# Kernel tuning notes

Hardware: AMD Instinct MI355X
Metric: run time of the kernel (lower is better)

Reference implementation:

```python
import jax, jax.numpy as jnp
import numpy as np

N_NODES = 100000
N_EDGES = 1600000
HIDDEN = 64
IN_CH = 6  # 3 (direction) + 3 (node feature part)
BN_EPS = 1e-5


def setup_inputs() -> dict:
    key = jax.random.key(0)
    ks = jax.random.split(key, 16)
    inp = {
        "x": jax.random.normal(ks[0], (N_NODES, 3), dtype=jnp.float32),
        "pos": jax.random.normal(ks[1], (N_NODES, 3), dtype=jnp.float32),
        "edge_index": jax.random.randint(ks[2], (2, N_EDGES), 0, N_NODES, dtype=jnp.int64),
    }
    dims = [IN_CH, HIDDEN, HIDDEN, HIDDEN]
    for i in range(3):
        din, dout = dims[i], dims[i + 1]
        inp[f"W{i+1}"] = jax.random.normal(ks[3 + 4 * i], (din, dout), dtype=jnp.float32) * (1.0 / np.sqrt(din))
        inp[f"b{i+1}"] = jnp.zeros((dout,), dtype=jnp.float32)
        inp[f"g{i+1}"] = jnp.ones((dout,), dtype=jnp.float32)   # BN gamma
        inp[f"be{i+1}"] = jnp.zeros((dout,), dtype=jnp.float32)  # BN beta
    return inp


def _mlp_layer(h, W, b, g, be):
    # Linear -> ReLU -> BatchNorm1d (training mode, biased variance like torch)
    h = jax.nn.relu(h @ W + b)
    mu = jnp.mean(h, axis=0)
    var = jnp.mean((h - mu) ** 2, axis=0)
    return g * (h - mu) * jax.lax.rsqrt(var + BN_EPS) + be


def reference(x, pos, edge_index, W1, b1, g1, be1, W2, b2, g2, be2, W3, b3, g3, be3):
    n = x.shape[0]
    xp = jnp.concatenate([pos, x], axis=1)             # [N, 3+F]
    src, dst = edge_index[0], edge_index[1]            # j = src, i = dst (PyG source_to_target)
    x_j = xp[src]                                      # [E, 3+F]
    x_i = xp[dst]
    direction = x_j[:, :3] - x_i[:, :3]                # [E, 3]
    # NOTE: source uses torch.norm with no dim => single global scalar norm
    direction = direction / jnp.linalg.norm(direction)
    h = jnp.concatenate([direction, x_i[:, 3:]], axis=-1)  # [E, IN_CH]
    h = _mlp_layer(h, W1, b1, g1, be1)
    h = _mlp_layer(h, W2, b2, g2, be2)
    h = _mlp_layer(h, W3, b3, g3, be3)                 # [E, HIDDEN]
    out = jax.ops.segment_max(h, dst, num_segments=n)  # scatter-max aggregation
    out = jnp.where(jnp.isfinite(out), out, 0.0)       # PyG fills empty segments with 0
    return out
```

## Files before the change

### kernel.cpp

```cpp
#include <hip/hip_runtime.h>
#include <stdint.h>

typedef unsigned short u16;
typedef unsigned int u32;
typedef __attribute__((ext_vector_type(8))) short short8;
typedef __attribute__((ext_vector_type(4))) float floatx4;

#define BN_EPS 1e-5f
#define NPB 64
#define NPB_SHIFT 6
#define NBMAX 2048

__device__ __forceinline__ float bf2f(u16 u) { return __uint_as_float(((unsigned)u) << 16); }
__device__ __forceinline__ u16 f2bf(float f) {
  unsigned u = __float_as_uint(f);
  u += 0x7FFFu + ((u >> 16) & 1u);
  return (u16)(u >> 16);
}

__global__ void k_init(float* __restrict__ stats, u32* __restrict__ bucketTotal) {
  for (int i = threadIdx.x; i < 1024; i += blockDim.x) stats[i] = 0.f;
  for (int i = threadIdx.x; i < NBMAX + 1; i += blockDim.x) bucketTotal[i] = 0u;
}

__global__ void k_norm_hist(const int* __restrict__ ei, const float* __restrict__ pos,
                            int E, int NB, float* __restrict__ stats,
                            u32* __restrict__ bucketTotal) {
  __shared__ u32 lh[NBMAX];
  __shared__ float red[16];
  for (int i = threadIdx.x; i < NB; i += blockDim.x) lh[i] = 0u;
  __syncthreads();
  int tid = blockIdx.x * blockDim.x + threadIdx.x;
  int stride = gridDim.x * blockDim.x;
  float acc = 0.f;
  for (int e = tid; e < E; e += stride) {
    int s = ei[e], d = ei[E + e];
    float d0 = pos[3 * s + 0] - pos[3 * d + 0];
    float d1 = pos[3 * s + 1] - pos[3 * d + 1];
    float d2 = pos[3 * s + 2] - pos[3 * d + 2];
    acc = fmaf(d0, d0, acc);
    acc = fmaf(d1, d1, acc);
    acc = fmaf(d2, d2, acc);
    atomicAdd(&lh[d >> NPB_SHIFT], 1u);
  }
#pragma unroll
  for (int off = 32; off > 0; off >>= 1) acc += __shfl_down(acc, off, 64);
  if ((threadIdx.x & 63) == 0) red[threadIdx.x >> 6] = acc;
  __syncthreads();
  if (threadIdx.x == 0) {
    float s = 0.f;
    for (int w = 0; w < (int)(blockDim.x >> 6); w++) s += red[w];
    atomicAdd(&stats[0], s);
  }
  for (int i = threadIdx.x; i < NB; i += blockDim.x)
    if (lh[i]) atomicAdd(&bucketTotal[i], lh[i]);
}

__global__ void k_scan(const u32* __restrict__ bucketTotal, u32* __restrict__ base,
                       u32* __restrict__ cursor, int NB) {
  int lane = threadIdx.x;
  u32 run = 0;
  for (int b0 = 0; b0 < NB; b0 += 64) {
    int b = b0 + lane;
    u32 v = (b < NB) ? bucketTotal[b] : 0u;
    u32 s = v;
#pragma unroll
    for (int off = 1; off < 64; off <<= 1) {
      u32 t = __shfl_up(s, off, 64);
      if (lane >= off) s += t;
    }
    u32 excl = run + s - v;
    if (b < NB) { base[b] = excl; cursor[b] = excl; }
    run += __shfl(s, 63, 64);
  }
  if (lane == 0) base[NB] = run;
}

__global__ void k_place(const int* __restrict__ ei, int E, int NB,
                        u32* __restrict__ cursor, u32* __restrict__ sorted) {
  __shared__ u32 lh[NBMAX];
  __shared__ u32 lbase[NBMAX];
  for (int i = threadIdx.x; i < NB; i += blockDim.x) lh[i] = 0u;
  __syncthreads();
  int tid = blockIdx.x * blockDim.x + threadIdx.x;
  int stride = gridDim.x * blockDim.x;
  for (int e = tid; e < E; e += stride) atomicAdd(&lh[ei[E + e] >> NPB_SHIFT], 1u);
  __syncthreads();
  for (int i = threadIdx.x; i < NB; i += blockDim.x) {
    u32 c = lh[i];
    lbase[i] = c ? atomicAdd(&cursor[i], c) : 0u;
    lh[i] = 0u;
  }
  __syncthreads();
  for (int e = tid; e < E; e += stride) {
    int d = ei[E + e];
    int b = d >> NPB_SHIFT;
    u32 slot = lbase[b] + atomicAdd(&lh[b], 1u);
    sorted[slot] = ((u32)e << 8) | (u32)(d & (NPB - 1));
  }
}

__global__ __launch_bounds__(256) void k_bucket_max(
    const u32* __restrict__ sorted, const u32* __restrict__ base,
    const u16* __restrict__ h, const float* __restrict__ gsum3,
    const float* __restrict__ gsq3, const float* __restrict__ g3,
    const float* __restrict__ be3, float invE, float* __restrict__ outf, int N) {
  __shared__ u32 tile[NPB * 64];
  for (int i = threadIdx.x; i < NPB * 64; i += blockDim.x) tile[i] = 0u;
  int b = blockIdx.x;
  u32 start = base[b];
  int cnt = (int)(base[b + 1] - start);
  int t = threadIdx.x;
  int es = t >> 3;
  int c0 = (t & 7) * 8;
  u32 mm[4];
#pragma unroll
  for (int p = 0; p < 4; p++) {
    u32 m0 = (g3[c0 + 2 * p] < 0.f) ? 0xFFFFu : 0u;
    u32 m1 = (g3[c0 + 2 * p + 1] < 0.f) ? 0xFFFFu : 0u;
    mm[p] = m0 | (m1 << 16);
  }
  __syncthreads();

  for (int i0 = 0; i0 < cnt; i0 += 128) {
    uint4 raw[4];
    u32 ln[4];
    int ok[4];
#pragma unroll
    for (int u_ = 0; u_ < 4; u_++) {
      int sl = i0 + u_ * 32 + es;
      ok[u_] = sl < cnt;
      if (ok[u_]) {
        ln[u_] = sorted[start + sl] & (u32)(NPB - 1);
        raw[u_] = *(const uint4*)(h + (long)(start + sl) * 64 + c0);
      }
    }
#pragma unroll
    for (int u_ = 0; u_ < 4; u_++) {
      if (!ok[u_]) continue;
      unsigned w[4] = {raw[u_].x, raw[u_].y, raw[u_].z, raw[u_].w};
      u32 key[8];
#pragma unroll
      for (int p = 0; p < 4; p++) {
        u32 wx = w[p] ^ mm[p];
        key[2 * p] = (wx & 0xFFFFu) | 0x10000u;
        key[2 * p + 1] = (wx >> 16) | 0x10000u;
      }
      u32 baseA = ln[u_] * 64u + (u32)c0;
#pragma unroll
      for (int jj = 0; jj < 8; jj++) {
        int j = (jj + es) & 7;
        atomicMax(&tile[baseA + j], key[j]);
      }
    }
  }
  __syncthreads();
  int c = t & 63;
  float mu = gsum3[c] * invE;
  float var = gsq3[c] * invE - mu * mu;
  float sc = g3[c] * rsqrtf(var + BN_EPS);
  float sh = be3[c] - mu * sc;
  u32 me = (g3[c] < 0.f) ? 0xFFFFu : 0u;
  int node0 = b * NPB;
  for (int l = t; l < NPB * 64; l += blockDim.x) {
    int node = node0 + (l >> 6);
    if (node < N) {
      u32 k = tile[l];
      float v = (k == 0u) ? 0.f : fmaf(bf2f((u16)((k & 0xFFFFu) ^ me)), sc, sh);
      outf[(long)node * 64 + (l & 63)] = v;
    }
  }
}

__global__ __launch_bounds__(256) void k_layer1(
    const int* __restrict__ ei, const float* __restrict__ pos,
    const float* __restrict__ x, const float* __restrict__ W1,
    const float* __restrict__ b1, u16* __restrict__ h,
    const float* __restrict__ stats, float* __restrict__ gsum,
    float* __restrict__ gsq, int E, const u32* __restrict__ sorted) {
  __shared__ float in6[6][256];
  __shared__ float ssum[64], ssq[64];
  float invn = 1.0f / sqrtf(stats[0]);
  int t = threadIdx.x;
  int lane = t & 63;
  int wv = t >> 6;
  float w[6];
#pragma unroll
  for (int k = 0; k < 6; k++) w[k] = W1[k * 64 + lane];
  float bias = b1[lane];
  float psum = 0.f, psq = 0.f;

  int chunks = (E + 255) >> 8;
  for (int c = blockIdx.x; c < chunks; c += gridDim.x) {
    long e0 = (long)c << 8;
    int e = (int)e0 + t;
    float v[6] = {0.f, 0.f, 0.f, 0.f, 0.f, 0.f};
    if (e < E) {
      int eid = sorted ? (int)(sorted[e] >> 8) : e;
      int s = ei[eid], d = ei[E + eid];
      float p0 = pos[3 * s + 0], p1 = pos[3 * s + 1], p2 = pos[3 * s + 2];
      float q0 = pos[3 * d + 0], q1 = pos[3 * d + 1], q2 = pos[3 * d + 2];
      v[0] = (p0 - q0) * invn;
      v[1] = (p1 - q1) * invn;
      v[2] = (p2 - q2) * invn;
      v[3] = x[3 * d + 0];
      v[4] = x[3 * d + 1];
      v[5] = x[3 * d + 2];
    }
    __syncthreads();
#pragma unroll
    for (int k = 0; k < 6; k++) in6[k][t] = v[k];
    __syncthreads();
    int lim = E - (int)e0;
    if (lim > 256) lim = 256;
    int base = wv * 64;
#pragma unroll 4
    for (int i = 0; i < 64; i++) {
      int el = base + i;
      if (el >= lim) break;
      float acc = bias;
#pragma unroll
      for (int k = 0; k < 6; k++) acc = fmaf(in6[k][el], w[k], acc);
      acc = fmaxf(acc, 0.f);
      u16 hb = f2bf(acc);
      h[(e0 + el) * 64 + lane] = hb;
      float hf = bf2f(hb);
      psum += hf;
      psq = fmaf(hf, hf, psq);
    }
  }
  if (t < 64) { ssum[t] = 0.f; ssq[t] = 0.f; }
  __syncthreads();
  atomicAdd(&ssum[lane], psum);
  atomicAdd(&ssq[lane], psq);
  __syncthreads();
  if (t < 64) {
    atomicAdd(&gsum[t], ssum[t]);
    atomicAdd(&gsq[t], ssq[t]);
  }
}

__global__ __launch_bounds__(256) void k_layer_mfma(
    u16* h, const float* __restrict__ W, const float* __restrict__ b,
    const float* __restrict__ gsum_in, const float* __restrict__ gsq_in,
    const float* __restrict__ g_in, const float* __restrict__ be_in, float invE,
    float* __restrict__ gsum, float* __restrict__ gsq, int E) {
  __shared__ float sc_s[64], sh_s[64];
  if (threadIdx.x < 64) {
    int c = threadIdx.x;
    float mu = gsum_in[c] * invE;
    float var = gsq_in[c] * invE - mu * mu;
    float s = g_in[c] * rsqrtf(var + BN_EPS);
    sc_s[c] = s;
    sh_s[c] = be_in[c] - mu * s;
  }
  __syncthreads();

  int lane = threadIdx.x & 63;
  int m = lane & 15;
  int q = lane >> 4;

  short8 bf[4][2];
  float bias[4];
#pragma unroll
  for (int t = 0; t < 4; t++) {
    int n = t * 16 + m;
    float bb = b[n];
    for (int k = 0; k < 64; k++) bb = fmaf(sh_s[k], W[k * 64 + n], bb);
    bias[t] = bb;
#pragma unroll
    for (int s = 0; s < 2; s++)
#pragma unroll
      for (int j = 0; j < 8; j++) {
        int k = s * 32 + q * 8 + j;
        bf[t][s][j] = (short)f2bf(W[k * 64 + n] * sc_s[k]);
      }
  }

  float psum[4] = {0.f, 0.f, 0.f, 0.f}, psq[4] = {0.f, 0.f, 0.f, 0.f};

  int tiles = E >> 4;
  int gw = ((int)blockIdx.x * (blockDim.x >> 6)) + (threadIdx.x >> 6);
  int nw = (int)gridDim.x * (blockDim.x >> 6);

  for (int tile = gw; tile < tiles; tile += nw) {
    long e0 = (long)tile * 16;
    const u16* rowp = h + (e0 + m) * 64 + q * 8;
    short8 a0 = *(const short8*)(rowp);
    short8 a1 = *(const short8*)(rowp + 32);
    floatx4 acc[4];
#pragma unroll
    for (int t = 0; t < 4; t++) acc[t] = (floatx4){0.f, 0.f, 0.f, 0.f};
#pragma unroll
    for (int t = 0; t < 4; t++)
      acc[t] = __builtin_amdgcn_mfma_f32_16x16x32_bf16(a0, bf[t][0], acc[t], 0, 0, 0);
#pragma unroll
    for (int t = 0; t < 4; t++)
      acc[t] = __builtin_amdgcn_mfma_f32_16x16x32_bf16(a1, bf[t][1], acc[t], 0, 0, 0);

#pragma unroll
    for (int t = 0; t < 4; t++) {
#pragma unroll
      for (int r = 0; r < 4; r++) {
        float v = acc[t][r] + bias[t];
        v = fmaxf(v, 0.f);
        u16 hb = f2bf(v);
        h[(e0 + q * 4 + r) * 64 + t * 16 + m] = hb;
        float hf = bf2f(hb);
        psum[t] += hf;
        psq[t] = fmaf(hf, hf, psq[t]);
      }
    }
  }

#pragma unroll
  for (int t = 0; t < 4; t++) {
    psum[t] += __shfl_xor(psum[t], 16, 64);
    psum[t] += __shfl_xor(psum[t], 32, 64);
    psq[t] += __shfl_xor(psq[t], 16, 64);
    psq[t] += __shfl_xor(psq[t], 32, 64);
  }
  __shared__ float ssum[64], ssq[64];
  if (threadIdx.x < 64) { ssum[threadIdx.x] = 0.f; ssq[threadIdx.x] = 0.f; }
  __syncthreads();
  if (q == 0) {
#pragma unroll
    for (int t = 0; t < 4; t++) {
      atomicAdd(&ssum[t * 16 + m], psum[t]);
      atomicAdd(&ssq[t * 16 + m], psq[t]);
    }
  }
  __syncthreads();
  if (threadIdx.x < 64) {
    atomicAdd(&gsum[threadIdx.x], ssum[threadIdx.x]);
    atomicAdd(&gsq[threadIdx.x], ssq[threadIdx.x]);
  }
}

__global__ void k_initout(float* __restrict__ outf, long n, float* __restrict__ stats,
                          u32* __restrict__ bucketTotal) {
  long i = (long)blockIdx.x * blockDim.x + threadIdx.x;
  long stride = (long)gridDim.x * blockDim.x;
  for (long j = i; j < n; j += stride) outf[j] = __uint_as_float(0xFF800000u);
  if (i < 1024) stats[i] = 0.f;
  if (i < NBMAX + 1) bucketTotal[i] = 0u;
}
__global__ void k_scatter(const int* __restrict__ ei, const u16* __restrict__ h,
                          const float* __restrict__ gsum3, const float* __restrict__ gsq3,
                          const float* __restrict__ g3, const float* __restrict__ be3,
                          float invE, float* outf, int E) {
  int lane = threadIdx.x & 63;
  int gw = ((int)blockIdx.x * (blockDim.x >> 6)) + (threadIdx.x >> 6);
  int nw = (int)gridDim.x * (blockDim.x >> 6);
  float mu = gsum3[lane] * invE;
  float var = gsq3[lane] * invE - mu * mu;
  float sc = g3[lane] * rsqrtf(var + BN_EPS);
  float sh = be3[lane] - mu * sc;
  for (int e = gw; e < E; e += nw) {
    int d = ei[E + e];
    float v = fmaf(bf2f(h[(long)e * 64 + lane]), sc, sh);
    float* addr = outf + (long)d * 64 + lane;
    if (v >= 0.f)
      atomicMax((int*)addr, __float_as_int(v));
    else
      atomicMin((unsigned int*)addr, __float_as_uint(v));
  }
}
__global__ void k_out(float* __restrict__ outf, long n) {
  long i = (long)blockIdx.x * blockDim.x + threadIdx.x;
  long stride = (long)gridDim.x * blockDim.x;
  for (long j = i; j < n; j += stride) {
    float v = outf[j];
    unsigned u = __float_as_uint(v);
    if ((u & 0x7F800000u) == 0x7F800000u) v = 0.f;
    outf[j] = v;
  }
}

extern "C" void kernel_launch(void* const* d_in, const int* in_sizes, int n_in,
                              void* d_out, int out_size, void* d_ws, size_t ws_size,
                              hipStream_t stream) {
  const float* x = (const float*)d_in[0];
  const float* pos = (const float*)d_in[1];
  const int* ei = (const int*)d_in[2];
  const float* W1 = (const float*)d_in[3];
  const float* b1 = (const float*)d_in[4];
  const float* g1 = (const float*)d_in[5];
  const float* be1 = (const float*)d_in[6];
  const float* W2 = (const float*)d_in[7];
  const float* b2 = (const float*)d_in[8];
  const float* g2 = (const float*)d_in[9];
  const float* be2 = (const float*)d_in[10];
  const float* W3 = (const float*)d_in[11];
  const float* b3 = (const float*)d_in[12];
  const float* g3 = (const float*)d_in[13];
  const float* be3 = (const float*)d_in[14];

  int N = in_sizes[0] / 3;
  int E = in_sizes[2] / 2;
  int NB = (N + NPB - 1) / NPB;
  long n_out = (long)N * 64;

  char* wsb = (char*)d_ws;
  u16* h = (u16*)wsb;
  size_t off = (size_t)E * 64 * 2;
  float* stats = (float*)(wsb + off);
  off += 1024 * 4;
  u32* bucketTotal = (u32*)(wsb + off);
  off += (NBMAX + 1) * 4;
  u32* baseArr = (u32*)(wsb + off);
  off += (NBMAX + 1) * 4;
  u32* cursor = (u32*)(wsb + off);
  off += NBMAX * 4;
  u32* sorted = (u32*)(wsb + off);
  off += (size_t)E * 4;
  size_t need = off;

  float* gsum1 = stats + 64, * gsq1 = stats + 128;
  float* gsum2 = stats + 192, * gsq2 = stats + 256;
  float* gsum3 = stats + 320, * gsq3 = stats + 384;

  float* outf = (float*)d_out;
  float invE = 1.0f / (float)E;
  bool binned = (ws_size >= need) && (NB <= NBMAX);

  if (binned) {
    k_init<<<1, 1024, 0, stream>>>(stats, bucketTotal);
    k_norm_hist<<<256, 256, 0, stream>>>(ei, pos, E, NB, stats, bucketTotal);
    k_scan<<<1, 64, 0, stream>>>(bucketTotal, baseArr, cursor, NB);
    k_place<<<256, 256, 0, stream>>>(ei, E, NB, cursor, sorted);
    k_layer1<<<1024, 256, 0, stream>>>(ei, pos, x, W1, b1, h, stats, gsum1, gsq1, E, sorted);
    k_layer_mfma<<<1024, 256, 0, stream>>>(h, W2, b2, gsum1, gsq1, g1, be1, invE, gsum2, gsq2, E);
    k_layer_mfma<<<1024, 256, 0, stream>>>(h, W3, b3, gsum2, gsq2, g2, be2, invE, gsum3, gsq3, E);
    k_bucket_max<<<NB, 256, 0, stream>>>(sorted, baseArr, h, gsum3, gsq3, g3, be3, invE, outf, N);
  } else {
    k_initout<<<4096, 256, 0, stream>>>(outf, n_out, stats, bucketTotal);
    k_norm_hist<<<256, 256, 0, stream>>>(ei, pos, E, NB <= NBMAX ? NB : 1, stats, bucketTotal);
    k_layer1<<<1024, 256, 0, stream>>>(ei, pos, x, W1, b1, h, stats, gsum1, gsq1, E, (const u32*)nullptr);
    k_layer_mfma<<<1024, 256, 0, stream>>>(h, W2, b2, gsum1, gsq1, g1, be1, invE, gsum2, gsq2, E);
    k_layer_mfma<<<1024, 256, 0, stream>>>(h, W3, b3, gsum2, gsq2, g2, be2, invE, gsum3, gsq3, E);
    k_scatter<<<2048, 256, 0, stream>>>(ei, h, gsum3, gsq3, g3, be3, invE, outf, E);
    k_out<<<2048, 256, 0, stream>>>(outf, n_out);
  }
}
```

Baseline: 495.4 us.

## Fuse layer-3 MFMA with bucketed segment-max and store (src,dst) pairs in sorted order

The third MLP layer is now computed per destination bucket, and its ReLU/bf16 outputs are max-reduced straight into a shared-memory tile. This removes the write and re-read of the layer-3 activations. Layer-3 BN statistics are still accumulated, and a new final pass applies the BN affine to the stored max keys, relying on the monotone sign-flip trick. The sort now stores (src,dst) pairs, so layer1 no longer does an indirect edge-index lookup, at the cost of doubling the sorted buffer. Risks include lower parallelism, since one block handles each 64-node bucket, and per-block bias recomputation over 64 k-terms.

```diff
diff --git a/kernel.cpp b/kernel.cpp
--- a/kernel.cpp
+++ b/kernel.cpp
@@ -77,7 +77,7 @@
 }
 
 __global__ void k_place(const int* __restrict__ ei, int E, int NB,
-                        u32* __restrict__ cursor, u32* __restrict__ sorted) {
+                        u32* __restrict__ cursor, uint2* __restrict__ sorted2) {
   __shared__ u32 lh[NBMAX];
   __shared__ u32 lbase[NBMAX];
   for (int i = threadIdx.x; i < NB; i += blockDim.x) lh[i] = 0u;
@@ -93,82 +93,11 @@
   }
   __syncthreads();
   for (int e = tid; e < E; e += stride) {
+    int s = ei[e];
     int d = ei[E + e];
     int b = d >> NPB_SHIFT;
     u32 slot = lbase[b] + atomicAdd(&lh[b], 1u);
-    sorted[slot] = ((u32)e << 8) | (u32)(d & (NPB - 1));
-  }
-}
-
-__global__ __launch_bounds__(256) void k_bucket_max(
-    const u32* __restrict__ sorted, const u32* __restrict__ base,
-    const u16* __restrict__ h, const float* __restrict__ gsum3,
-    const float* __restrict__ gsq3, const float* __restrict__ g3,
-    const float* __restrict__ be3, float invE, float* __restrict__ outf, int N) {
-  __shared__ u32 tile[NPB * 64];
-  for (int i = threadIdx.x; i < NPB * 64; i += blockDim.x) tile[i] = 0u;
-  int b = blockIdx.x;
-  u32 start = base[b];
-  int cnt = (int)(base[b + 1] - start);
-  int t = threadIdx.x;
-  int es = t >> 3;
-  int c0 = (t & 7) * 8;
-  u32 mm[4];
-#pragma unroll
-  for (int p = 0; p < 4; p++) {
-    u32 m0 = (g3[c0 + 2 * p] < 0.f) ? 0xFFFFu : 0u;
-    u32 m1 = (g3[c0 + 2 * p + 1] < 0.f) ? 0xFFFFu : 0u;
-    mm[p] = m0 | (m1 << 16);
-  }
-  __syncthreads();
-
-  for (int i0 = 0; i0 < cnt; i0 += 128) {
-    uint4 raw[4];
-    u32 ln[4];
-    int ok[4];
-#pragma unroll
-    for (int u_ = 0; u_ < 4; u_++) {
-      int sl = i0 + u_ * 32 + es;
-      ok[u_] = sl < cnt;
-      if (ok[u_]) {
-        ln[u_] = sorted[start + sl] & (u32)(NPB - 1);
-        raw[u_] = *(const uint4*)(h + (long)(start + sl) * 64 + c0);
-      }
-    }
-#pragma unroll
-    for (int u_ = 0; u_ < 4; u_++) {
-      if (!ok[u_]) continue;
-      unsigned w[4] = {raw[u_].x, raw[u_].y, raw[u_].z, raw[u_].w};
-      u32 key[8];
-#pragma unroll
-      for (int p = 0; p < 4; p++) {
-        u32 wx = w[p] ^ mm[p];
-        key[2 * p] = (wx & 0xFFFFu) | 0x10000u;
-        key[2 * p + 1] = (wx >> 16) | 0x10000u;
-      }
-      u32 baseA = ln[u_] * 64u + (u32)c0;
-#pragma unroll
-      for (int jj = 0; jj < 8; jj++) {
-        int j = (jj + es) & 7;
-        atomicMax(&tile[baseA + j], key[j]);
-      }
-    }
-  }
-  __syncthreads();
-  int c = t & 63;
-  float mu = gsum3[c] * invE;
-  float var = gsq3[c] * invE - mu * mu;
-  float sc = g3[c] * rsqrtf(var + BN_EPS);
-  float sh = be3[c] - mu * sc;
-  u32 me = (g3[c] < 0.f) ? 0xFFFFu : 0u;
-  int node0 = b * NPB;
-  for (int l = t; l < NPB * 64; l += blockDim.x) {
-    int node = node0 + (l >> 6);
-    if (node < N) {
-      u32 k = tile[l];
-      float v = (k == 0u) ? 0.f : fmaf(bf2f((u16)((k & 0xFFFFu) ^ me)), sc, sh);
-      outf[(long)node * 64 + (l & 63)] = v;
-    }
+    sorted2[slot] = make_uint2((u32)s, (u32)d);
   }
 }
 
@@ -177,7 +106,7 @@
     const float* __restrict__ x, const float* __restrict__ W1,
     const float* __restrict__ b1, u16* __restrict__ h,
     const float* __restrict__ stats, float* __restrict__ gsum,
-    float* __restrict__ gsq, int E, const u32* __restrict__ sorted) {
+    float* __restrict__ gsq, int E, const uint2* __restrict__ sorted2) {
   __shared__ float in6[6][256];
   __shared__ float ssum[64], ssq[64];
   float invn = 1.0f / sqrtf(stats[0]);
@@ -196,8 +125,15 @@
     int e = (int)e0 + t;
     float v[6] = {0.f, 0.f, 0.f, 0.f, 0.f, 0.f};
     if (e < E) {
-      int eid = sorted ? (int)(sorted[e] >> 8) : e;
-      int s = ei[eid], d = ei[E + eid];
+      int s, d;
+      if (sorted2) {
+        uint2 sd = sorted2[e];
+        s = (int)sd.x;
+        d = (int)sd.y;
+      } else {
+        s = ei[e];
+        d = ei[E + e];
+      }
       float p0 = pos[3 * s + 0], p1 = pos[3 * s + 1], p2 = pos[3 * s + 2];
       float q0 = pos[3 * d + 0], q1 = pos[3 * d + 1], q2 = pos[3 * d + 2];
       v[0] = (p0 - q0) * invn;
@@ -334,6 +270,152 @@
   if (threadIdx.x < 64) {
     atomicAdd(&gsum[threadIdx.x], ssum[threadIdx.x]);
     atomicAdd(&gsq[threadIdx.x], ssq[threadIdx.x]);
+  }
+}
+
+__global__ __launch_bounds__(256) void k_layer3_max(
+    const u16* __restrict__ h, const uint2* __restrict__ sorted2,
+    const u32* __restrict__ base, const float* __restrict__ W,
+    const float* __restrict__ b, const float* __restrict__ gsum_in,
+    const float* __restrict__ gsq_in, const float* __restrict__ g_in,
+    const float* __restrict__ be_in, float invE, float* __restrict__ gsum,
+    float* __restrict__ gsq, const float* __restrict__ g3,
+    u32* __restrict__ outk, int N) {
+  __shared__ float sc_s[64], sh_s[64];
+  __shared__ u32 tile[64 * 65];
+  __shared__ float ssum[64], ssq[64];
+  if (threadIdx.x < 64) {
+    int c = threadIdx.x;
+    float mu = gsum_in[c] * invE;
+    float var = gsq_in[c] * invE - mu * mu;
+    float s = g_in[c] * rsqrtf(var + BN_EPS);
+    sc_s[c] = s;
+    sh_s[c] = be_in[c] - mu * s;
+    ssum[c] = 0.f;
+    ssq[c] = 0.f;
+  }
+  for (int i = threadIdx.x; i < 64 * 65; i += blockDim.x) tile[i] = 0u;
+  __syncthreads();
+
+  int lane = threadIdx.x & 63;
+  int m = lane & 15;
+  int q = lane >> 4;
+  int wv = threadIdx.x >> 6;
+
+  short8 bf[4][2];
+  float bias[4];
+  u32 xmask[4];
+#pragma unroll
+  for (int t = 0; t < 4; t++) {
+    int n = t * 16 + m;
+    float bb = b[n];
+    for (int k = 0; k < 64; k++) bb = fmaf(sh_s[k], W[k * 64 + n], bb);
+    bias[t] = bb;
+    xmask[t] = (g3[n] < 0.f) ? 0xFFFFu : 0u;
+#pragma unroll
+    for (int s = 0; s < 2; s++)
+#pragma unroll
+      for (int j = 0; j < 8; j++) {
+        int k = s * 32 + q * 8 + j;
+        bf[t][s][j] = (short)f2bf(W[k * 64 + n] * sc_s[k]);
+      }
+  }
+
+  int bb_ = blockIdx.x;
+  int start = (int)base[bb_];
+  int end = (int)base[bb_ + 1];
+  float psum[4] = {0.f, 0.f, 0.f, 0.f}, psq[4] = {0.f, 0.f, 0.f, 0.f};
+
+  for (int i0 = start + wv * 16; i0 < end; i0 += 64) {
+    int rr = i0 + m;
+    if (rr > end - 1) rr = end - 1;
+    const u16* rowp = h + (long)rr * 64 + q * 8;
+    short8 a0 = *(const short8*)(rowp);
+    short8 a1 = *(const short8*)(rowp + 32);
+    floatx4 acc[4];
+#pragma unroll
+    for (int t = 0; t < 4; t++) acc[t] = (floatx4){0.f, 0.f, 0.f, 0.f};
+#pragma unroll
+    for (int t = 0; t < 4; t++)
+      acc[t] = __builtin_amdgcn_mfma_f32_16x16x32_bf16(a0, bf[t][0], acc[t], 0, 0, 0);
+#pragma unroll
+    for (int t = 0; t < 4; t++)
+      acc[t] = __builtin_amdgcn_mfma_f32_16x16x32_bf16(a1, bf[t][1], acc[t], 0, 0, 0);
+
+    u32 lnr[4];
+#pragma unroll
+    for (int r = 0; r < 4; r++) {
+      int sl = i0 + q * 4 + r;
+      lnr[r] = (sl < end) ? (sorted2[sl].y & (u32)(NPB - 1)) : 0xFFFFFFFFu;
+    }
+#pragma unroll
+    for (int t = 0; t < 4; t++) {
+      int c = t * 16 + m;
+      u32 curln = 0xFFFFFFFFu, curkey = 0u;
+#pragma unroll
+      for (int r = 0; r < 4; r++) {
+        if (lnr[r] == 0xFFFFFFFFu) continue;
+        float v = acc[t][r] + bias[t];
+        v = fmaxf(v, 0.f);
+        u16 hb = f2bf(v);
+        float hf = bf2f(hb);
+        psum[t] += hf;
+        psq[t] = fmaf(hf, hf, psq[t]);
+        u32 key = ((u32)hb ^ xmask[t]) | 0x10000u;
+        if (lnr[r] == curln) {
+          curkey = key > curkey ? key : curkey;
+        } else {
+          if (curln != 0xFFFFFFFFu) atomicMax(&tile[curln * 65 + c], curkey);
+          curln = lnr[r];
+          curkey = key;
+        }
+      }
+      if (curln != 0xFFFFFFFFu) atomicMax(&tile[curln * 65 + c], curkey);
+    }
+  }
+
+#pragma unroll
+  for (int t = 0; t < 4; t++) {
+    psum[t] += __shfl_xor(psum[t], 16, 64);
+    psum[t] += __shfl_xor(psum[t], 32, 64);
+    psq[t] += __shfl_xor(psq[t], 16, 64);
+    psq[t] += __shfl_xor(psq[t], 32, 64);
+  }
+  __syncthreads();
+  if (q == 0) {
+#pragma unroll
+    for (int t = 0; t < 4; t++) {
+      atomicAdd(&ssum[t * 16 + m], psum[t]);
+      atomicAdd(&ssq[t * 16 + m], psq[t]);
+    }
+  }
+  __syncthreads();
+  if (threadIdx.x < 64) {
+    if (ssum[threadIdx.x] != 0.f) atomicAdd(&gsum[threadIdx.x], ssum[threadIdx.x]);
+    if (ssq[threadIdx.x] != 0.f) atomicAdd(&gsq[threadIdx.x], ssq[threadIdx.x]);
+  }
+  int node0 = bb_ * NPB;
+  for (int l = threadIdx.x; l < NPB * 64; l += blockDim.x) {
+    int node = node0 + (l >> 6);
+    if (node < N) outk[(long)node * 64 + (l & 63)] = tile[(l >> 6) * 65 + (l & 63)];
+  }
+}
+
+__global__ void k_final(u32* __restrict__ outk, const float* __restrict__ gsum3,
+                        const float* __restrict__ gsq3, const float* __restrict__ g3,
+                        const float* __restrict__ be3, float invE, long n) {
+  int c = threadIdx.x & 63;
+  float mu = gsum3[c] * invE;
+  float var = gsq3[c] * invE - mu * mu;
+  float sc = g3[c] * rsqrtf(var + BN_EPS);
+  float sh = be3[c] - mu * sc;
+  u32 me = (g3[c] < 0.f) ? 0xFFFFu : 0u;
+  long i = (long)blockIdx.x * blockDim.x + threadIdx.x;
+  long stride = (long)gridDim.x * blockDim.x;
+  for (long j = i; j < n; j += stride) {
+    u32 k = outk[j];
+    float v = (k == 0u) ? 0.f : fmaf(bf2f((u16)((k & 0xFFFFu) ^ me)), sc, sh);
+    ((float*)outk)[j] = v;
   }
 }
 
@@ -412,8 +494,9 @@
   off += (NBMAX + 1) * 4;
   u32* cursor = (u32*)(wsb + off);
   off += NBMAX * 4;
-  u32* sorted = (u32*)(wsb + off);
-  off += (size_t)E * 4;
+  off = (off + 7) & ~(size_t)7;
+  uint2* sorted2 = (uint2*)(wsb + off);
+  off += (size_t)E * 8;
   size_t need = off;
 
   float* gsum1 = stats + 64, * gsq1 = stats + 128;
@@ -428,15 +511,16 @@
     k_init<<<1, 1024, 0, stream>>>(stats, bucketTotal);
     k_norm_hist<<<256, 256, 0, stream>>>(ei, pos, E, NB, stats, bucketTotal);
     k_scan<<<1, 64, 0, stream>>>(bucketTotal, baseArr, cursor, NB);
-    k_place<<<256, 256, 0, stream>>>(ei, E, NB, cursor, sorted);
-    k_layer1<<<1024, 256, 0, stream>>>(ei, pos, x, W1, b1, h, stats, gsum1, gsq1, E, sorted);
+    k_place<<<256, 256, 0, stream>>>(ei, E, NB, cursor, sorted2);
+    k_layer1<<<1024, 256, 0, stream>>>(ei, pos, x, W1, b1, h, stats, gsum1, gsq1, E, sorted2);
     k_layer_mfma<<<1024, 256, 0, stream>>>(h, W2, b2, gsum1, gsq1, g1, be1, invE, gsum2, gsq2, E);
-    k_layer_mfma<<<1024, 256, 0, stream>>>(h, W3, b3, gsum2, gsq2, g2, be2, invE, gsum3, gsq3, E);
-    k_bucket_max<<<NB, 256, 0, stream>>>(sorted, baseArr, h, gsum3, gsq3, g3, be3, invE, outf, N);
+    k_layer3_max<<<NB, 256, 0, stream>>>(h, sorted2, baseArr, W3, b3, gsum2, gsq2, g2, be2,
+                                         invE, gsum3, gsq3, g3, (u32*)outf, N);
+    k_final<<<1024, 256, 0, stream>>>((u32*)outf, gsum3, gsq3, g3, be3, invE, n_out);
   } else {
     k_initout<<<4096, 256, 0, stream>>>(outf, n_out, stats, bucketTotal);
     k_norm_hist<<<256, 256, 0, stream>>>(ei, pos, E, NB <= NBMAX ? NB : 1, stats, bucketTotal);
-    k_layer1<<<1024, 256, 0, stream>>>(ei, pos, x, W1, b1, h, stats, gsum1, gsq1, E, (const u32*)nullptr);
+    k_layer1<<<1024, 256, 0, stream>>>(ei, pos, x, W1, b1, h, stats, gsum1, gsq1, E, (const uint2*)nullptr);
     k_layer_mfma<<<1024, 256, 0, stream>>>(h, W2, b2, gsum1, gsq1, g1, be1, invE, gsum2, gsq2, E);
     k_layer_mfma<<<1024, 256, 0, stream>>>(h, W3, b3, gsum2, gsq2, g2, be2, invE, gsum3, gsq3, E);
     k_scatter<<<2048, 256, 0, stream>>>(ei, h, gsum3, gsq3, g3, be3, invE, outf, E);
```

Result: no change. 499.4 us (+0.8%).
